# Performance work log

Measured on AMD Instinct MI355X. Metric: run time of the kernel, lower is better.

Reference implementation:

```python
import jax, jax.numpy as jnp
import numpy as np

N = 25000   # num nodes
E = 500000  # num edges
B = 4       # num queries (batch)
D = 32      # hidden dim
R2 = 474    # doubled num_relation
L = 4       # num conv layers
EPS = 1e-6


def setup_inputs() -> dict:
    key = jax.random.key(0)
    ks = jax.random.split(key, 12)
    return {
        "node_in": jax.random.randint(ks[0], (E,), 0, N),
        "node_out": jax.random.randint(ks[1], (E,), 0, N),
        "relation": jax.random.randint(ks[2], (E,), 0, R2),
        "edge_weight": jnp.ones((E,), jnp.float32),
        "h_index": jax.random.randint(ks[3], (B,), 0, N),
        "r_index": jax.random.randint(ks[4], (B,), 0, R2),
        "query_embed": jax.random.normal(ks[5], (R2, D), jnp.float32) * 0.1,
        "rel_W": jax.random.normal(ks[6], (L, D, R2 * D), jnp.float32) * 0.05,
        "rel_b": jnp.zeros((L, R2 * D), jnp.float32),
        "lin_W": jax.random.normal(ks[7], (L, 13 * D, D), jnp.float32) * 0.05,
        "lin_b": jnp.zeros((L, D), jnp.float32),
        "mlp_W1": jax.random.normal(ks[8], (2 * D, 2 * D), jnp.float32) * 0.05,
        "mlp_b1": jnp.zeros((2 * D,), jnp.float32),
        "mlp_W2": jax.random.normal(ks[9], (2 * D, 1), jnp.float32) * 0.05,
        "mlp_b2": jnp.zeros((1,), jnp.float32),
    }


def _nbfnet(node_in, node_out, relation, h_index, r_index,
            edge_weight, query_embed, rel_W, rel_b, lin_W, lin_b,
            mlp_W1, mlp_b1, mlp_W2, mlp_b2):
    query = query_embed[r_index]                                   # [B, D]
    # boundary condition: query embedding placed at the head node of each query
    boundary = jnp.zeros((N, B, D), query.dtype).at[h_index, jnp.arange(B)].set(query)
    # append one self-entry per node (boundary message), as in the torch code
    node_out_ext = jnp.concatenate([node_out, jnp.arange(N)])      # [E+N]
    w_ext = jnp.concatenate([edge_weight, jnp.ones((N,), edge_weight.dtype)])[:, None, None]
    cnt = jax.ops.segment_sum(jnp.ones((E + N,), query.dtype), node_out_ext, N)[:, None, None]
    deg = jax.ops.segment_sum(edge_weight, node_out, N) + 1.0      # degree_out + 1, [N]
    scale = jnp.log(deg)
    scale = scale / scale.mean()
    scales = jnp.stack([jnp.ones_like(scale), scale, 1.0 / jnp.clip(scale, 0.01)], -1)  # [N,3]

    hidden = boundary
    for l in range(L):
        # dependent relation embeddings: [R2, B, D]
        rel_in = (query @ rel_W[l] + rel_b[l]).reshape(B, R2, D).transpose(1, 0, 2)
        # distmult message + boundary self-message: [E+N, B, D]
        msg = jnp.concatenate([rel_in[relation] * hidden[node_in], boundary], 0)
        mw = msg * w_ext
        mean = jax.ops.segment_sum(mw, node_out_ext, N) / cnt
        sq_mean = jax.ops.segment_sum(msg * mw, node_out_ext, N) / cnt
        mx = jax.ops.segment_max(mw, node_out_ext, N)
        mn = jax.ops.segment_min(mw, node_out_ext, N)
        std = jnp.sqrt(jnp.clip(sq_mean - mean * mean, EPS))
        feat = jnp.stack([mean, mx, mn, std], -1).reshape(N, B, 4 * D)   # PNA stats
        update = (feat[..., None] * scales[:, None, None, :]).reshape(N, B, 12 * D)
        hidden = jax.nn.relu(jnp.concatenate([hidden, update], -1) @ lin_W[l] + lin_b[l])

    feat = jnp.concatenate([hidden, jnp.broadcast_to(query[None], (N, B, D))], -1)  # [N,B,2D]
    h1 = jax.nn.relu(feat @ mlp_W1 + mlp_b1)
    score = (h1 @ mlp_W2 + mlp_b2)[..., 0]                          # [N, B]
    return score.T                                                  # [B, N]


def reference(node_in, node_out, relation, edge_weight, h_index, r_index,
              query_embed, rel_W, rel_b, lin_W, lin_b,
              mlp_W1, mlp_b1, mlp_W2, mlp_b2):
    return _nbfnet(node_in, node_out, relation, h_index, r_index,
                   edge_weight, query_embed, rel_W, rel_b, lin_W, lin_b,
                   mlp_W1, mlp_b1, mlp_W2, mlp_b2)
```

## Files before the change

kernel.cpp:

```cpp
#include <hip/hip_runtime.h>
#include <hip/hip_fp16.h>

#define NN  25000
#define EE  500000
#define BB  4
#define DD  32
#define LL  4
#define R2C 474
#define BD  128
#define THD 416
#define EPSF 1e-6f
#define WMH 13312

typedef _Float16 half8 __attribute__((ext_vector_type(8)));
typedef float    f32x4 __attribute__((ext_vector_type(4)));

__global__ __launch_bounds__(256) void pidx_kernel(const int4* __restrict__ no4,
                                                   int* __restrict__ cnt,
                                                   int4* __restrict__ pidx4) {
  int i = blockIdx.x * 256 + threadIdx.x;
  if (i >= EE / 4) return;
  int4 d = no4[i];
  int4 r;
  r.x = atomicAdd(&cnt[d.x], 1);
  r.y = atomicAdd(&cnt[d.y], 1);
  r.z = atomicAdd(&cnt[d.z], 1);
  r.w = atomicAdd(&cnt[d.w], 1);
  pidx4[i] = r;
}

__global__ __launch_bounds__(256) void prep_kernel(const int* __restrict__ cnt,
                                                   int* __restrict__ base,
                                                   float* __restrict__ cntf,
                                                   int* __restrict__ gcnt) {
  int n = blockIdx.x * 256 + threadIdx.x;
  if (n >= NN) return;
  int c = cnt[n];
  base[n] = atomicAdd(gcnt, (c + 1) & ~1);
  cntf[n] = (float)(c + 1);
}

__global__ __launch_bounds__(256) void scatter_kernel(const int4* __restrict__ ni4,
                                                      const int4* __restrict__ no4,
                                                      const int4* __restrict__ rl4,
                                                      const float4* __restrict__ ew4,
                                                      const int* __restrict__ base,
                                                      const int4* __restrict__ pidx4,
                                                      int2* __restrict__ ep) {
  int i = blockIdx.x * 256 + threadIdx.x;
  if (i >= EE / 4) return;
  int4 ni = ni4[i], no = no4[i], rl = rl4[i], pi = pidx4[i];
  float4 w = ew4[i];
  ep[base[no.x] + pi.x] = make_int2(ni.x | (rl.x << 15), __float_as_int(w.x));
  ep[base[no.y] + pi.y] = make_int2(ni.y | (rl.y << 15), __float_as_int(w.y));
  ep[base[no.z] + pi.z] = make_int2(ni.z | (rl.z << 15), __float_as_int(w.z));
  ep[base[no.w] + pi.w] = make_int2(ni.w | (rl.w << 15), __float_as_int(w.w));
}

__global__ __launch_bounds__(256) void wdeg_kernel(const int* __restrict__ base,
                                                   const int* __restrict__ cnt,
                                                   const int2* __restrict__ ep,
                                                   float* __restrict__ lg,
                                                   float* __restrict__ logsum) {
  int n = blockIdx.x * 256 + threadIdx.x;
  float v = 0.f;
  if (n < NN) {
    int b = base[n], c = cnt[n];
    float s = 0.f;
    for (int p = b; p < b + c; ++p) s += __int_as_float(ep[p].y);
    v = logf(s + 1.0f);
    lg[n] = v;
  }
  __shared__ float red[256];
  red[threadIdx.x] = v; __syncthreads();
  for (int o = 128; o > 0; o >>= 1) {
    if (threadIdx.x < o) red[threadIdx.x] += red[threadIdx.x + o];
    __syncthreads();
  }
  if (threadIdx.x == 0) atomicAdd(logsum, red[0]);
}

__global__ __launch_bounds__(128) void init_kernel(const int* __restrict__ h_index,
                                                   const int* __restrict__ r_index,
                                                   const float* __restrict__ qemb,
                                                   float* __restrict__ query,
                                                   __half* __restrict__ h0) {
  int t = threadIdx.x; int b = t >> 5, d = t & 31;
  float qv = qemb[r_index[b] * DD + d];
  query[t] = qv;
  h0[h_index[b] * BD + t] = __float2half(qv);
}

__global__ __launch_bounds__(256) void relin_all_kernel(const float* __restrict__ query,
                                                        const float* __restrict__ relW,
                                                        const float* __restrict__ relB,
                                                        __half* __restrict__ relIn) {
  int o = blockIdx.x * 256 + threadIdx.x;
  if (o >= LL * R2C * BD) return;
  int l = o / (R2C * BD);
  int rest = o % (R2C * BD);
  int r = rest >> 7, b = (rest >> 5) & 3, d = rest & 31;
  int col = r * DD + d;
  const float* W = relW + (size_t)l * DD * R2C * DD;
  float acc = relB[(size_t)l * R2C * DD + col];
  #pragma unroll
  for (int k = 0; k < DD; ++k)
    acc = fmaf(query[b * DD + k], W[(size_t)k * (R2C * DD) + col], acc);
  relIn[o] = __float2half(acc);
}

__global__ __launch_bounds__(256) void wmbuild_kernel(const float* __restrict__ linW,
                                                      _Float16* __restrict__ Wm) {
  int idx = blockIdx.x * 256 + threadIdx.x;
  if (idx >= LL * WMH) return;
  int l = idx / WMH, rest = idx % WMH;
  int t = rest >> 10;
  int nt = (rest >> 9) & 1;
  int L = (rest >> 3) & 63;
  int j = rest & 7;
  int k = t * 32 + (L >> 4) * 8 + j;
  int n = nt * 16 + (L & 15);
  int wrow;
  if (k < 32) wrow = k;
  else {
    int kk = k - 32;
    int slab = kk >> 7, s = (kk >> 5) & 3, dd = kk & 31;
    wrow = DD + (dd * 4 + s) * 3 + slab;
  }
  Wm[idx] = (_Float16)linW[(size_t)l * THD * DD + (size_t)wrow * DD + n];
}

__global__ __launch_bounds__(256) void gather1_kernel(const __half2* __restrict__ rel2,
                                                      const int2* __restrict__ ep,
                                                      const int* __restrict__ base,
                                                      const int* __restrict__ cnt,
                                                      const float* __restrict__ cntf,
                                                      const int* __restrict__ h_index,
                                                      const float* __restrict__ query,
                                                      __half2* __restrict__ statsH) {
  const int lane = threadIdx.x & 63;
  const int n = blockIdx.x * 4 + (threadIdx.x >> 6);
  const int b = lane >> 4;
  const int d0 = (lane & 15) * 2;
  const float q0 = query[b * 32 + d0], q1 = query[b * 32 + d0 + 1];
  const int hb = h_index[b];
  const int beg = __builtin_amdgcn_readfirstlane(base[n]);
  const int cnn = __builtin_amdgcn_readfirstlane(cnt[n]);
  const float mb0 = (n == hb) ? q0 : 0.f;
  const float mb1 = (n == hb) ? q1 : 0.f;
  float sa0 = mb0, qa0 = mb0 * mb0, mx0 = mb0, mn0 = mb0;
  float sa1 = mb1, qa1 = mb1 * mb1, mx1 = mb1, mn1 = mb1;
  int matched = 0;
  for (int p = beg; p < beg + cnn; ++p) {
    int2 e = ep[p];
    int src = e.x & 0x7fff;
    if (src == hb) {
      __half2 rv = rel2[(unsigned)((unsigned)e.x >> 15) * 64 + lane];
      float w = __int_as_float(e.y);
      float2 rf = __half22float2(rv);
      float m0 = rf.x * q0, mw0 = m0 * w;
      float m1 = rf.y * q1, mw1 = m1 * w;
      sa0 += mw0; qa0 = fmaf(m0, mw0, qa0); mx0 = fmaxf(mx0, mw0); mn0 = fminf(mn0, mw0);
      sa1 += mw1; qa1 = fmaf(m1, mw1, qa1); mx1 = fmaxf(mx1, mw1); mn1 = fminf(mn1, mw1);
      ++matched;
    }
  }
  if (matched < cnn) {
    mx0 = fmaxf(mx0, 0.f); mn0 = fminf(mn0, 0.f);
    mx1 = fmaxf(mx1, 0.f); mn1 = fminf(mn1, 0.f);
  }
  const float invc = 1.0f / cntf[n];
  const float mean0 = sa0 * invc, mean1 = sa1 * invc;
  const float sd0 = sqrtf(fmaxf(qa0 * invc - mean0 * mean0, EPSF));
  const float sd1 = sqrtf(fmaxf(qa1 * invc - mean1 * mean1, EPSF));
  __half2* sp = statsH + (unsigned)n * 256 + lane;
  sp[0]   = __floats2half2_rn(mean0, mean1);
  sp[64]  = __floats2half2_rn(mx0, mx1);
  sp[128] = __floats2half2_rn(mn0, mn1);
  sp[192] = __floats2half2_rn(sd0, sd1);
}

__global__ __launch_bounds__(256) void gather_kernel(const __half2* __restrict__ hin2,
                                                     const __half2* __restrict__ rel2,
                                                     const int2* __restrict__ ep,
                                                     const int* __restrict__ base,
                                                     const int* __restrict__ cnt,
                                                     const float* __restrict__ cntf,
                                                     const int* __restrict__ h_index,
                                                     const float* __restrict__ query,
                                                     __half2* __restrict__ statsH) {
  const int lane = threadIdx.x & 63;
  const int n = blockIdx.x * 4 + (threadIdx.x >> 6);
  const int b = lane >> 4;
  const int d0 = (lane & 15) * 2;
  const float q0 = query[b * 32 + d0], q1 = query[b * 32 + d0 + 1];
  const int hb = h_index[b];
  const int beg = __builtin_amdgcn_readfirstlane(base[n]);
  const int cnn = __builtin_amdgcn_readfirstlane(cnt[n]);
  const float mb0 = (n == hb) ? q0 : 0.f;
  const float mb1 = (n == hb) ? q1 : 0.f;
  float sa0 = mb0, qa0 = mb0 * mb0, mx0 = mb0, mn0 = mb0;
  float sa1 = mb1, qa1 = mb1 * mb1, mx1 = mb1, mn1 = mb1;

#define PROC(Ez, Hv, Rv) {                                                   \
    float w = __int_as_float(Ez);                                            \
    float2 hf = __half22float2(Hv), rf = __half22float2(Rv);                 \
    float m0 = rf.x * hf.x, mw0 = m0 * w;                                    \
    float m1 = rf.y * hf.y, mw1 = m1 * w;                                    \
    sa0 += mw0; qa0 = fmaf(m0, mw0, qa0);                                    \
    mx0 = fmaxf(mx0, mw0); mn0 = fminf(mn0, mw0);                            \
    sa1 += mw1; qa1 = fmaf(m1, mw1, qa1);                                    \
    mx1 = fmaxf(mx1, mw1); mn1 = fminf(mn1, mw1); }
#define ROWS(Ex, Hd, Rd) {                                                   \
    Hd = hin2[(unsigned)((Ex) & 0x7fff) * 64 + lane];                        \
    Rd = rel2[(unsigned)((unsigned)(Ex) >> 15) * 64 + lane]; }

  int p = beg;
  int rem = cnn;
  const int nb = rem >> 3;
  if (nb > 0) {
    int2 E0, E1, E2, E3, E4, E5, E6, E7;
    __half2 H0, H1, H2, H3, H4, H5, H6, H7;
    __half2 R0, R1, R2, R3, R4, R5, R6, R7;
    E0 = ep[p];     E1 = ep[p + 1]; E2 = ep[p + 2]; E3 = ep[p + 3];
    E4 = ep[p + 4]; E5 = ep[p + 5]; E6 = ep[p + 6]; E7 = ep[p + 7];
    ROWS(E0.x, H0, R0); ROWS(E1.x, H1, R1); ROWS(E2.x, H2, R2); ROWS(E3.x, H3, R3);
    ROWS(E4.x, H4, R4); ROWS(E5.x, H5, R5); ROWS(E6.x, H6, R6); ROWS(E7.x, H7, R7);
    for (int it = 1; it < nb; ++it) {
      const int pn = p + 8;
      int2 F0 = ep[pn],     F1 = ep[pn + 1], F2 = ep[pn + 2], F3 = ep[pn + 3];
      int2 F4 = ep[pn + 4], F5 = ep[pn + 5], F6 = ep[pn + 6], F7 = ep[pn + 7];
      __half2 G0, G1, G2, G3, G4, G5, G6, G7;
      __half2 S0, S1, S2, S3, S4, S5, S6, S7;
      ROWS(F0.x, G0, S0); ROWS(F1.x, G1, S1); ROWS(F2.x, G2, S2); ROWS(F3.x, G3, S3);
      ROWS(F4.x, G4, S4); ROWS(F5.x, G5, S5); ROWS(F6.x, G6, S6); ROWS(F7.x, G7, S7);
      PROC(E0.y, H0, R0); PROC(E1.y, H1, R1); PROC(E2.y, H2, R2); PROC(E3.y, H3, R3);
      PROC(E4.y, H4, R4); PROC(E5.y, H5, R5); PROC(E6.y, H6, R6); PROC(E7.y, H7, R7);
      E0 = F0; E1 = F1; E2 = F2; E3 = F3; E4 = F4; E5 = F5; E6 = F6; E7 = F7;
      H0 = G0; H1 = G1; H2 = G2; H3 = G3; H4 = G4; H5 = G5; H6 = G6; H7 = G7;
      R0 = S0; R1 = S1; R2 = S2; R3 = S3; R4 = S4; R5 = S5; R6 = S6; R7 = S7;
      p = pn;
    }
    PROC(E0.y, H0, R0); PROC(E1.y, H1, R1); PROC(E2.y, H2, R2); PROC(E3.y, H3, R3);
    PROC(E4.y, H4, R4); PROC(E5.y, H5, R5); PROC(E6.y, H6, R6); PROC(E7.y, H7, R7);
    p += 8;
    rem -= nb << 3;
  }
  if (rem >= 4) {
    int2 E0 = ep[p], E1 = ep[p + 1], E2 = ep[p + 2], E3 = ep[p + 3];
    __half2 H0, H1, H2, H3, R0, R1, R2, R3;
    ROWS(E0.x, H0, R0); ROWS(E1.x, H1, R1); ROWS(E2.x, H2, R2); ROWS(E3.x, H3, R3);
    PROC(E0.y, H0, R0); PROC(E1.y, H1, R1); PROC(E2.y, H2, R2); PROC(E3.y, H3, R3);
    p += 4; rem -= 4;
  }
  for (; rem > 0; --rem, ++p) {
    int2 e = ep[p];
    __half2 hv, rv;
    ROWS(e.x, hv, rv);
    PROC(e.y, hv, rv);
  }
#undef ROWS
#undef PROC
  const float invc = 1.0f / cntf[n];
  const float mean0 = sa0 * invc, mean1 = sa1 * invc;
  const float sd0 = sqrtf(fmaxf(qa0 * invc - mean0 * mean0, EPSF));
  const float sd1 = sqrtf(fmaxf(qa1 * invc - mean1 * mean1, EPSF));
  __half2* sp = statsH + (unsigned)n * 256 + lane;
  sp[0]   = __floats2half2_rn(mean0, mean1);
  sp[64]  = __floats2half2_rn(mx0, mx1);
  sp[128] = __floats2half2_rn(mn0, mn1);
  sp[192] = __floats2half2_rn(sd0, sd1);
}

__global__ __launch_bounds__(128) void mfma_linear_kernel(const _Float16* __restrict__ hinh,
                                                          __half* __restrict__ houth,
                                                          const _Float16* __restrict__ statsH,
                                                          const float* __restrict__ lg,
                                                          const float* __restrict__ logsum,
                                                          const _Float16* __restrict__ Wm,
                                                          const float* __restrict__ bias) {
  const int lane = threadIdx.x & 63;
  const int wid  = threadIdx.x >> 6;
  const int nbase = blockIdx.x * 8 + wid * 4;
  const int m = lane & 15;
  const int q = lane >> 4;
  const int n = nbase + (m >> 2);
  const int b = m & 3;
  const float invmean = (float)NN / logsum[0];
  const float sc = lg[n] * invmean;
  const _Float16 one = (_Float16)1.f;
  const _Float16 s1h = (_Float16)sc;
  const _Float16 s2h = (_Float16)(1.0f / fmaxf(sc, 0.01f));
  const _Float16* hsrc = hinh   + (unsigned)n * BD  + b * 32 + q * 8;
  const _Float16* ssrc = statsH + (unsigned)n * 512 + b * 32 + q * 8;

  f32x4 c0 = {0.f, 0.f, 0.f, 0.f};
  f32x4 c1 = {0.f, 0.f, 0.f, 0.f};
  #pragma unroll
  for (int t = 0; t < 13; ++t) {
    half8 a;
    if (t == 0) {
      a = *(const half8*)hsrc;
    } else {
      const int slab = (t - 1) >> 2, s = (t - 1) & 3;
      a = *(const half8*)(ssrc + s * 128);
      const _Float16 sch = (slab == 0) ? one : ((slab == 1) ? s1h : s2h);
      half8 sv = {sch, sch, sch, sch, sch, sch, sch, sch};
      a = a * sv;
    }
    half8 b0 = *(const half8*)(Wm + (unsigned)(t * 2 + 0) * 512 + lane * 8);
    half8 b1 = *(const half8*)(Wm + (unsigned)(t * 2 + 1) * 512 + lane * 8);
    c0 = __builtin_amdgcn_mfma_f32_16x16x32_f16(a, b0, c0, 0, 0, 0);
    c1 = __builtin_amdgcn_mfma_f32_16x16x32_f16(a, b1, c1, 0, 0, 0);
  }
  const int col = lane & 15;
  const float bj0 = bias[col], bj1 = bias[col + 16];
  #pragma unroll
  for (int i = 0; i < 4; ++i) {
    const int mr = q * 4 + i;
    const int nl = mr >> 2, bq = mr & 3;
    __half* dst = houth + (unsigned)(nbase + nl) * BD + bq * 32 + col;
    dst[0]  = __float2half(fmaxf(c0[i] + bj0, 0.f));
    dst[16] = __float2half(fmaxf(c1[i] + bj1, 0.f));
  }
}

__global__ __launch_bounds__(128) void mlp_kernel(const __half* __restrict__ hinh,
                                                  const float* __restrict__ query,
                                                  const float* __restrict__ W1,
                                                  const float* __restrict__ b1,
                                                  const float* __restrict__ W2,
                                                  const float* __restrict__ b2,
                                                  float* __restrict__ out) {
  __shared__ float f2[BB][2 * DD];
  const int t = threadIdx.x;
  const int b = t >> 5, d = t & 31;
  const float qv = query[t];
  const float w2a = W2[d], w2b = W2[DD + d];
  const float b1a = b1[d], b1b = b1[DD + d];
  const float b2v = b2[0];
  const int NPBM = 8;
  int n0 = blockIdx.x * NPBM, n1 = min(n0 + NPBM, NN);
  for (int n = n0; n < n1; ++n) {
    f2[b][d]      = __half2float(hinh[(unsigned)n * BD + t]);
    f2[b][DD + d] = qv;
    float a0 = b1a, a1 = b1b;
    #pragma unroll
    for (int i = 0; i < 2 * DD; ++i) {
      float v = f2[b][i];
      a0 = fmaf(v, W1[i * 2 * DD + d], a0);
      a1 = fmaf(v, W1[i * 2 * DD + DD + d], a1);
    }
    a0 = fmaxf(a0, 0.f); a1 = fmaxf(a1, 0.f);
    float part = a0 * w2a + a1 * w2b;
    #pragma unroll
    for (int off = 16; off > 0; off >>= 1) part += __shfl_down(part, off, 32);
    if (d == 0) out[b * NN + n] = part + b2v;
  }
}

extern "C" void kernel_launch(void* const* d_in, const int* in_sizes, int n_in,
                              void* d_out, int out_size, void* d_ws, size_t ws_size,
                              hipStream_t stream) {
  const int*   node_in  = (const int*)d_in[0];
  const int*   node_out = (const int*)d_in[1];
  const int*   relation = (const int*)d_in[2];
  const float* ew       = (const float*)d_in[3];
  const int*   h_index  = (const int*)d_in[4];
  const int*   r_index  = (const int*)d_in[5];
  const float* qemb     = (const float*)d_in[6];
  const float* relW     = (const float*)d_in[7];
  const float* relB     = (const float*)d_in[8];
  const float* linW     = (const float*)d_in[9];
  const float* linB     = (const float*)d_in[10];
  const float* W1       = (const float*)d_in[11];
  const float* b1       = (const float*)d_in[12];
  const float* W2       = (const float*)d_in[13];
  const float* b2       = (const float*)d_in[14];
  float* out = (float*)d_out;

  char* ws = (char*)d_ws;
  size_t off = 0;
  auto alloc = [&](size_t bytes) -> char* {
    char* p = ws + off;
    off += (bytes + 255) & ~(size_t)255;
    return p;
  };
  __half*   h0     = (__half*)  alloc((size_t)NN * BD * 2);
  __half*   h1     = (__half*)  alloc((size_t)NN * BD * 2);
  __half*   relIn  = (__half*)  alloc((size_t)LL * R2C * BD * 2);
  __half*   statsH = (__half*)  alloc((size_t)NN * 512 * 2);
  _Float16* Wm     = (_Float16*)alloc((size_t)LL * WMH * 2);
  int2*     ep     = (int2*)    alloc(((size_t)EE + NN) * 8);
  int*      pidx   = (int*)     alloc((size_t)EE * 4);
  int*      base   = (int*)     alloc((size_t)NN * 4);
  int*      cnti   = (int*)     alloc((size_t)NN * 4);
  float*    lg     = (float*)   alloc((size_t)NN * 4);
  float*    cntf   = (float*)   alloc((size_t)NN * 4);
  float*    query  = (float*)   alloc((size_t)BD * 4);
  float*    stats  = (float*)   alloc(256);

  hipMemsetAsync(cnti, 0, (size_t)NN * 4, stream);
  hipMemsetAsync(stats, 0, 256, stream);
  hipMemsetAsync(h0,   0, (size_t)NN * BD * 2, stream);

  float* logsum = stats;
  int*   gcnt   = (int*)stats + 1;

  pidx_kernel   <<<(EE / 4 + 255) / 256, 256, 0, stream>>>((const int4*)node_out,
                                                           cnti, (int4*)pidx);
  prep_kernel   <<<(NN + 255) / 256, 256, 0, stream>>>(cnti, base, cntf, gcnt);
  scatter_kernel<<<(EE / 4 + 255) / 256, 256, 0, stream>>>(
      (const int4*)node_in, (const int4*)node_out, (const int4*)relation,
      (const float4*)ew, base, (const int4*)pidx, ep);
  wdeg_kernel   <<<(NN + 255) / 256, 256, 0, stream>>>(base, cnti, ep, lg, logsum);
  init_kernel   <<<1, 128, 0, stream>>>(h_index, r_index, qemb, query, h0);
  wmbuild_kernel<<<(LL * WMH + 255) / 256, 256, 0, stream>>>(linW, Wm);
  relin_all_kernel<<<(LL * R2C * BD + 255) / 256, 256, 0, stream>>>(query, relW, relB, relIn);

  __half* hin = h0; __half* hout = h1;
  for (int l = 0; l < LL; ++l) {
    if (l == 0) {
      gather1_kernel<<<NN / 4, 256, 0, stream>>>(
          (const __half2*)relIn, ep, base, cnti, cntf, h_index, query,
          (__half2*)statsH);
    } else {
      gather_kernel<<<NN / 4, 256, 0, stream>>>(
          (const __half2*)hin, (const __half2*)relIn + (size_t)l * R2C * 64,
          ep, base, cnti, cntf, h_index, query, (__half2*)statsH);
    }
    mfma_linear_kernel<<<NN / 8, 128, 0, stream>>>(
        (const _Float16*)hin, hout, (const _Float16*)statsH, lg, logsum,
        Wm + (size_t)l * WMH, linB + (size_t)l * DD);
    __half* tmp = hin; hin = hout; hout = tmp;
  }
  mlp_kernel<<<(NN + 7) / 8, 128, 0, stream>>>(hin, query, W1, b1, W2, b2, out);
}
```

Measured before the change: 302.5 us.

## Fuse gather statistics and MFMA linear into one per-layer kernel via LDS

Each layer's gather kernel now writes its PNA statistics to shared memory, and the first wave of the block then runs the MFMA linear epilogue directly. This removes the global statsH round trip and one launch per layer. Layer 1 builds the boundary input on the fly instead of reading a zeroed h0, which drops the h0 memset and the cntf array. The cost is that three of the four waves sit idle during the MFMA epilogue, and blocks are smaller (4 nodes per block instead of 8).

```diff
diff --git a/kernel.cpp b/kernel.cpp
--- a/kernel.cpp
+++ b/kernel.cpp
@@ -31,13 +31,10 @@
 
 __global__ __launch_bounds__(256) void prep_kernel(const int* __restrict__ cnt,
                                                    int* __restrict__ base,
-                                                   float* __restrict__ cntf,
                                                    int* __restrict__ gcnt) {
   int n = blockIdx.x * 256 + threadIdx.x;
   if (n >= NN) return;
-  int c = cnt[n];
-  base[n] = atomicAdd(gcnt, (c + 1) & ~1);
-  cntf[n] = (float)(c + 1);
+  base[n] = atomicAdd(gcnt, (cnt[n] + 1) & ~1);
 }
 
 __global__ __launch_bounds__(256) void scatter_kernel(const int4* __restrict__ ni4,
@@ -80,15 +77,11 @@
   if (threadIdx.x == 0) atomicAdd(logsum, red[0]);
 }
 
-__global__ __launch_bounds__(128) void init_kernel(const int* __restrict__ h_index,
-                                                   const int* __restrict__ r_index,
+__global__ __launch_bounds__(128) void init_kernel(const int* __restrict__ r_index,
                                                    const float* __restrict__ qemb,
-                                                   float* __restrict__ query,
-                                                   __half* __restrict__ h0) {
+                                                   float* __restrict__ query) {
   int t = threadIdx.x; int b = t >> 5, d = t & 31;
-  float qv = qemb[r_index[b] * DD + d];
-  query[t] = qv;
-  h0[h_index[b] * BD + t] = __float2half(qv);
+  query[t] = qemb[r_index[b] * DD + d];
 }
 
 __global__ __launch_bounds__(256) void relin_all_kernel(const float* __restrict__ query,
@@ -130,16 +123,77 @@
   Wm[idx] = (_Float16)linW[(size_t)l * THD * DD + (size_t)wrow * DD + n];
 }
 
-__global__ __launch_bounds__(256) void gather1_kernel(const __half2* __restrict__ rel2,
-                                                      const int2* __restrict__ ep,
-                                                      const int* __restrict__ base,
-                                                      const int* __restrict__ cnt,
-                                                      const float* __restrict__ cntf,
-                                                      const int* __restrict__ h_index,
-                                                      const float* __restrict__ query,
-                                                      __half2* __restrict__ statsH) {
+__device__ __forceinline__ void mfma_epilogue(const _Float16* sh,
+                                              const _Float16* hinh,
+                                              __half* houth,
+                                              const float* lg,
+                                              const float* logsum,
+                                              const _Float16* Wm,
+                                              const float* bias,
+                                              const float* query,
+                                              const int* h_index,
+                                              int nbase, int lane, bool hzero) {
+  const int m = lane & 15;
+  const int q = lane >> 4;
+  const int nl = m >> 2;
+  const int n = nbase + nl;
+  const int b = m & 3;
+  const float sc = lg[n] * ((float)NN / logsum[0]);
+  const _Float16 one = (_Float16)1.f;
+  const _Float16 s1h = (_Float16)sc;
+  const _Float16 s2h = (_Float16)(1.0f / fmaxf(sc, 0.01f));
+  const _Float16* ssrc = sh + nl * 512 + b * 32 + q * 8;
+
+  f32x4 c0 = {0.f, 0.f, 0.f, 0.f};
+  f32x4 c1 = {0.f, 0.f, 0.f, 0.f};
+  half8 a;
+  if (hzero) {
+    a = (half8)(_Float16)0.f;
+    if (n == h_index[b]) {
+      const float* qp = query + b * 32 + q * 8;
+      #pragma unroll
+      for (int j = 0; j < 8; ++j) a[j] = (_Float16)qp[j];
+    }
+  } else {
+    a = *(const half8*)(hinh + (unsigned)n * BD + b * 32 + q * 8);
+  }
+  #pragma unroll
+  for (int t = 0; t < 13; ++t) {
+    if (t > 0) {
+      const int slab = (t - 1) >> 2, s = (t - 1) & 3;
+      a = *(const half8*)(ssrc + s * 128);
+      const _Float16 sch = (slab == 0) ? one : ((slab == 1) ? s1h : s2h);
+      half8 sv = {sch, sch, sch, sch, sch, sch, sch, sch};
+      a = a * sv;
+    }
+    half8 b0 = *(const half8*)(Wm + (unsigned)(t * 2 + 0) * 512 + lane * 8);
+    half8 b1 = *(const half8*)(Wm + (unsigned)(t * 2 + 1) * 512 + lane * 8);
+    c0 = __builtin_amdgcn_mfma_f32_16x16x32_f16(a, b0, c0, 0, 0, 0);
+    c1 = __builtin_amdgcn_mfma_f32_16x16x32_f16(a, b1, c1, 0, 0, 0);
+  }
+  const int col = lane & 15;
+  const float bj0 = bias[col], bj1 = bias[col + 16];
+  #pragma unroll
+  for (int i = 0; i < 4; ++i) {
+    const int mr = q * 4 + i;
+    __half* dst = houth + (unsigned)(nbase + (mr >> 2)) * BD + (mr & 3) * 32 + col;
+    dst[0]  = __float2half(fmaxf(c0[i] + bj0, 0.f));
+    dst[16] = __float2half(fmaxf(c1[i] + bj1, 0.f));
+  }
+}
+
+__global__ __launch_bounds__(256) void layer1_fused_kernel(
+    const __half2* __restrict__ rel2, const int2* __restrict__ ep,
+    const int* __restrict__ base, const int* __restrict__ cnt,
+    const int* __restrict__ h_index, const float* __restrict__ query,
+    const float* __restrict__ lg, const float* __restrict__ logsum,
+    const _Float16* __restrict__ Wm, const float* __restrict__ bias,
+    __half* __restrict__ houth) {
+  __shared__ __align__(16) __half2 sh[4][256];
   const int lane = threadIdx.x & 63;
-  const int n = blockIdx.x * 4 + (threadIdx.x >> 6);
+  const int wid  = threadIdx.x >> 6;
+  const int nbase = blockIdx.x * 4;
+  const int n = nbase + wid;
   const int b = lane >> 4;
   const int d0 = (lane & 15) * 2;
   const float q0 = query[b * 32 + d0], q1 = query[b * 32 + d0 + 1];
@@ -153,8 +207,7 @@
   int matched = 0;
   for (int p = beg; p < beg + cnn; ++p) {
     int2 e = ep[p];
-    int src = e.x & 0x7fff;
-    if (src == hb) {
+    if ((e.x & 0x7fff) == hb) {
       __half2 rv = rel2[(unsigned)((unsigned)e.x >> 15) * 64 + lane];
       float w = __int_as_float(e.y);
       float2 rf = __half22float2(rv);
@@ -169,28 +222,32 @@
     mx0 = fmaxf(mx0, 0.f); mn0 = fminf(mn0, 0.f);
     mx1 = fmaxf(mx1, 0.f); mn1 = fminf(mn1, 0.f);
   }
-  const float invc = 1.0f / cntf[n];
+  const float invc = 1.0f / (float)(cnn + 1);
   const float mean0 = sa0 * invc, mean1 = sa1 * invc;
   const float sd0 = sqrtf(fmaxf(qa0 * invc - mean0 * mean0, EPSF));
   const float sd1 = sqrtf(fmaxf(qa1 * invc - mean1 * mean1, EPSF));
-  __half2* sp = statsH + (unsigned)n * 256 + lane;
-  sp[0]   = __floats2half2_rn(mean0, mean1);
-  sp[64]  = __floats2half2_rn(mx0, mx1);
-  sp[128] = __floats2half2_rn(mn0, mn1);
-  sp[192] = __floats2half2_rn(sd0, sd1);
-}
-
-__global__ __launch_bounds__(256) void gather_kernel(const __half2* __restrict__ hin2,
-                                                     const __half2* __restrict__ rel2,
-                                                     const int2* __restrict__ ep,
-                                                     const int* __restrict__ base,
-                                                     const int* __restrict__ cnt,
-                                                     const float* __restrict__ cntf,
-                                                     const int* __restrict__ h_index,
-                                                     const float* __restrict__ query,
-                                                     __half2* __restrict__ statsH) {
+  sh[wid][lane]       = __floats2half2_rn(mean0, mean1);
+  sh[wid][64 + lane]  = __floats2half2_rn(mx0, mx1);
+  sh[wid][128 + lane] = __floats2half2_rn(mn0, mn1);
+  sh[wid][192 + lane] = __floats2half2_rn(sd0, sd1);
+  __syncthreads();
+  if (threadIdx.x >= 64) return;
+  mfma_epilogue((const _Float16*)&sh[0][0], nullptr, houth, lg, logsum,
+                Wm, bias, query, h_index, nbase, lane, true);
+}
+
+__global__ __launch_bounds__(256) void layer_fused_kernel(
+    const __half2* __restrict__ hin2, const __half2* __restrict__ rel2,
+    const int2* __restrict__ ep, const int* __restrict__ base,
+    const int* __restrict__ cnt, const int* __restrict__ h_index,
+    const float* __restrict__ query, const float* __restrict__ lg,
+    const float* __restrict__ logsum, const _Float16* __restrict__ Wm,
+    const float* __restrict__ bias, __half* __restrict__ houth) {
+  __shared__ __align__(16) __half2 sh[4][256];
   const int lane = threadIdx.x & 63;
-  const int n = blockIdx.x * 4 + (threadIdx.x >> 6);
+  const int wid  = threadIdx.x >> 6;
+  const int nbase = blockIdx.x * 4;
+  const int n = nbase + wid;
   const int b = lane >> 4;
   const int d0 = (lane & 15) * 2;
   const float q0 = query[b * 32 + d0], q1 = query[b * 32 + d0 + 1];
@@ -261,68 +318,18 @@
   }
 #undef ROWS
 #undef PROC
-  const float invc = 1.0f / cntf[n];
+  const float invc = 1.0f / (float)(cnn + 1);
   const float mean0 = sa0 * invc, mean1 = sa1 * invc;
   const float sd0 = sqrtf(fmaxf(qa0 * invc - mean0 * mean0, EPSF));
   const float sd1 = sqrtf(fmaxf(qa1 * invc - mean1 * mean1, EPSF));
-  __half2* sp = statsH + (unsigned)n * 256 + lane;
-  sp[0]   = __floats2half2_rn(mean0, mean1);
-  sp[64]  = __floats2half2_rn(mx0, mx1);
-  sp[128] = __floats2half2_rn(mn0, mn1);
-  sp[192] = __floats2half2_rn(sd0, sd1);
-}
-
-__global__ __launch_bounds__(128) void mfma_linear_kernel(const _Float16* __restrict__ hinh,
-                                                          __half* __restrict__ houth,
-                                                          const _Float16* __restrict__ statsH,
-                                                          const float* __restrict__ lg,
-                                                          const float* __restrict__ logsum,
-                                                          const _Float16* __restrict__ Wm,
-                                                          const float* __restrict__ bias) {
-  const int lane = threadIdx.x & 63;
-  const int wid  = threadIdx.x >> 6;
-  const int nbase = blockIdx.x * 8 + wid * 4;
-  const int m = lane & 15;
-  const int q = lane >> 4;
-  const int n = nbase + (m >> 2);
-  const int b = m & 3;
-  const float invmean = (float)NN / logsum[0];
-  const float sc = lg[n] * invmean;
-  const _Float16 one = (_Float16)1.f;
-  const _Float16 s1h = (_Float16)sc;
-  const _Float16 s2h = (_Float16)(1.0f / fmaxf(sc, 0.01f));
-  const _Float16* hsrc = hinh   + (unsigned)n * BD  + b * 32 + q * 8;
-  const _Float16* ssrc = statsH + (unsigned)n * 512 + b * 32 + q * 8;
-
-  f32x4 c0 = {0.f, 0.f, 0.f, 0.f};
-  f32x4 c1 = {0.f, 0.f, 0.f, 0.f};
-  #pragma unroll
-  for (int t = 0; t < 13; ++t) {
-    half8 a;
-    if (t == 0) {
-      a = *(const half8*)hsrc;
-    } else {
-      const int slab = (t - 1) >> 2, s = (t - 1) & 3;
-      a = *(const half8*)(ssrc + s * 128);
-      const _Float16 sch = (slab == 0) ? one : ((slab == 1) ? s1h : s2h);
-      half8 sv = {sch, sch, sch, sch, sch, sch, sch, sch};
-      a = a * sv;
-    }
-    half8 b0 = *(const half8*)(Wm + (unsigned)(t * 2 + 0) * 512 + lane * 8);
-    half8 b1 = *(const half8*)(Wm + (unsigned)(t * 2 + 1) * 512 + lane * 8);
-    c0 = __builtin_amdgcn_mfma_f32_16x16x32_f16(a, b0, c0, 0, 0, 0);
-    c1 = __builtin_amdgcn_mfma_f32_16x16x32_f16(a, b1, c1, 0, 0, 0);
-  }
-  const int col = lane & 15;
-  const float bj0 = bias[col], bj1 = bias[col + 16];
-  #pragma unroll
-  for (int i = 0; i < 4; ++i) {
-    const int mr = q * 4 + i;
-    const int nl = mr >> 2, bq = mr & 3;
-    __half* dst = houth + (unsigned)(nbase + nl) * BD + bq * 32 + col;
-    dst[0]  = __float2half(fmaxf(c0[i] + bj0, 0.f));
-    dst[16] = __float2half(fmaxf(c1[i] + bj1, 0.f));
-  }
+  sh[wid][lane]       = __floats2half2_rn(mean0, mean1);
+  sh[wid][64 + lane]  = __floats2half2_rn(mx0, mx1);
+  sh[wid][128 + lane] = __floats2half2_rn(mn0, mn1);
+  sh[wid][192 + lane] = __floats2half2_rn(sd0, sd1);
+  __syncthreads();
+  if (threadIdx.x >= 64) return;
+  mfma_epilogue((const _Float16*)&sh[0][0], (const _Float16*)hin2, houth,
+                lg, logsum, Wm, bias, query, h_index, nbase, lane, false);
 }
 
 __global__ __launch_bounds__(128) void mlp_kernel(const __half* __restrict__ hinh,
@@ -389,49 +396,44 @@
   __half*   h0     = (__half*)  alloc((size_t)NN * BD * 2);
   __half*   h1     = (__half*)  alloc((size_t)NN * BD * 2);
   __half*   relIn  = (__half*)  alloc((size_t)LL * R2C * BD * 2);
-  __half*   statsH = (__half*)  alloc((size_t)NN * 512 * 2);
   _Float16* Wm     = (_Float16*)alloc((size_t)LL * WMH * 2);
   int2*     ep     = (int2*)    alloc(((size_t)EE + NN) * 8);
   int*      pidx   = (int*)     alloc((size_t)EE * 4);
   int*      base   = (int*)     alloc((size_t)NN * 4);
   int*      cnti   = (int*)     alloc((size_t)NN * 4);
   float*    lg     = (float*)   alloc((size_t)NN * 4);
-  float*    cntf   = (float*)   alloc((size_t)NN * 4);
   float*    query  = (float*)   alloc((size_t)BD * 4);
   float*    stats  = (float*)   alloc(256);
 
   hipMemsetAsync(cnti, 0, (size_t)NN * 4, stream);
   hipMemsetAsync(stats, 0, 256, stream);
-  hipMemsetAsync(h0,   0, (size_t)NN * BD * 2, stream);
 
   float* logsum = stats;
   int*   gcnt   = (int*)stats + 1;
 
   pidx_kernel   <<<(EE / 4 + 255) / 256, 256, 0, stream>>>((const int4*)node_out,
                                                            cnti, (int4*)pidx);
-  prep_kernel   <<<(NN + 255) / 256, 256, 0, stream>>>(cnti, base, cntf, gcnt);
+  prep_kernel   <<<(NN + 255) / 256, 256, 0, stream>>>(cnti, base, gcnt);
   scatter_kernel<<<(EE / 4 + 255) / 256, 256, 0, stream>>>(
       (const int4*)node_in, (const int4*)node_out, (const int4*)relation,
       (const float4*)ew, base, (const int4*)pidx, ep);
   wdeg_kernel   <<<(NN + 255) / 256, 256, 0, stream>>>(base, cnti, ep, lg, logsum);
-  init_kernel   <<<1, 128, 0, stream>>>(h_index, r_index, qemb, query, h0);
+  init_kernel   <<<1, 128, 0, stream>>>(r_index, qemb, query);
   wmbuild_kernel<<<(LL * WMH + 255) / 256, 256, 0, stream>>>(linW, Wm);
   relin_all_kernel<<<(LL * R2C * BD + 255) / 256, 256, 0, stream>>>(query, relW, relB, relIn);
 
   __half* hin = h0; __half* hout = h1;
   for (int l = 0; l < LL; ++l) {
     if (l == 0) {
-      gather1_kernel<<<NN / 4, 256, 0, stream>>>(
-          (const __half2*)relIn, ep, base, cnti, cntf, h_index, query,
-          (__half2*)statsH);
+      layer1_fused_kernel<<<NN / 4, 256, 0, stream>>>(
+          (const __half2*)relIn, ep, base, cnti, h_index, query, lg, logsum,
+          Wm, linB, hout);
     } else {
-      gather_kernel<<<NN / 4, 256, 0, stream>>>(
+      layer_fused_kernel<<<NN / 4, 256, 0, stream>>>(
           (const __half2*)hin, (const __half2*)relIn + (size_t)l * R2C * 64,
-          ep, base, cnti, cntf, h_index, query, (__half2*)statsH);
-    }
-    mfma_linear_kernel<<<NN / 8, 128, 0, stream>>>(
-        (const _Float16*)hin, hout, (const _Float16*)statsH, lg, logsum,
-        Wm + (size_t)l * WMH, linB + (size_t)l * DD);
+          ep, base, cnti, h_index, query, lg, logsum,
+          Wm + (size_t)l * WMH, linB + (size_t)l * DD, hout);
+    }
     __half* tmp = hin; hin = hout; hout = tmp;
   }
   mlp_kernel<<<(NN + 7) / 8, 128, 0, stream>>>(hin, query, W1, b1, W2, b2, out);
```

New measurement: 288.5 us. -4.6%, faster.
